# Performance work log

Measured on AMD Instinct MI355X. Metric: run time of the kernel, lower is better.

## Reference

```python
import jax, jax.numpy as jnp
import numpy as np

N = 16384
C_IN = 128
C_OUT = 128
S_DIM = 4
P_DIM = 32
K = 16


def setup_inputs() -> dict:
    key = jax.random.key(0)
    ks = jax.random.split(key, 8)
    lim = lambda fan_in: 1.0 / np.sqrt(fan_in)
    u = lambda k_, shape, b: jax.random.uniform(k_, shape, jnp.float32, -b, b)
    return {
        "x": jax.random.normal(ks[0], (N, C_IN), jnp.float32),
        "Ws": u(ks[1], (S_DIM, C_IN), lim(C_IN)),
        "bs": u(ks[2], (S_DIM,), lim(C_IN)),
        "Wh": u(ks[3], (P_DIM, C_IN), lim(C_IN)),
        "bh": u(ks[4], (P_DIM,), lim(C_IN)),
        "W1": u(ks[5], (C_OUT, C_IN), lim(C_IN)),
        "W2": u(ks[6], (C_OUT, 2 * P_DIM), lim(2 * P_DIM)),
        "b2": u(ks[7], (C_OUT,), lim(2 * P_DIM)),
        "k": K,
    }


def reference(x, Ws, bs, Wh, bh, W1, W2, b2, k):
    # latent space positions and message vectors
    s = x @ Ws.T + bs            # [N, S]
    h = x @ Wh.T + bh            # [N, P]
    # squared-distance matrix via Gram trick (monotone in true distance,
    # so k-NN indices match torch.cdist + topk(largest=False))
    sq = jnp.sum(s * s, axis=-1)                         # [N]
    d2 = sq[:, None] + sq[None, :] - 2.0 * (s @ s.T)     # [N, N]
    _, idx = jax.lax.top_k(-d2, k)                       # [N, k] neighbour ids (incl. self)
    # exact squared latent distance to selected neighbours (as in torch code)
    s_j = s[idx]                                          # [N, k, S]
    w = jnp.exp(-10.0 * jnp.sum((s[:, None, :] - s_j) ** 2, axis=-1))  # [N, k]
    msg = h[idx] * w[..., None]                           # [N, k, P]
    agg = jnp.concatenate([msg.mean(axis=1), msg.max(axis=1)], axis=-1)  # [N, 2P]
    return x @ W1.T + agg @ W2.T + b2                     # [N, C_OUT]
```

## Files before the change

### kernel.cpp

```cpp
#include <hip/hip_runtime.h>
#include <hip/hip_bf16.h>


#define NPTS 16384
#define CIN  128
#define SD   4
#define PD   32
#define KNN  16
#define COUT 128
#define FLTMAX 3.4028234663852886e+38f
#define NBIN 33
#define QPB  8
#define QCAP 512
#define MCAP 128
#define EPAD 1e-3f

typedef float v2f __attribute__((ext_vector_type(2)));
typedef unsigned int uint;
typedef unsigned long long u64;
typedef unsigned short u16;
typedef __attribute__((ext_vector_type(8))) short bf16x8;
typedef __attribute__((ext_vector_type(4))) float f32x4;

#define WS_S4     0
#define WS_H      0x40000
#define WS_AGG_M  0x280000
#define WS_SA     0x280000
#define WS_SB     0x300000
#define WS_WT_M   0x680000
#define WS_T2     0x6A0000
#define WS_MASK   0x700000
#define WS_NEED_M 0x2700000
#define WS_CJ_F   0x400000
#define WS_AGG_F  0xC00000
#define WS_WT_F   0x1000000
#define JS   16
#define TJF  (NPTS/JS)

__device__ __forceinline__ float d2f(const float4 a, const float4 b) {
  v2f d0 = {a.x - b.x, a.y - b.y};
  v2f d1 = {a.z - b.z, a.w - b.w};
  v2f pr = d0*d0 + d1*d1;
  return pr.x + pr.y;
}

__device__ __forceinline__ u16 f2bf(float x) {
  uint u = __float_as_uint(x);
  uint r = (u + 0x7FFFu + ((u >> 16) & 1u)) >> 16;
  return (u16)r;
}
__device__ __forceinline__ float bf2f(u16 h) {
  return __uint_as_float(((uint)h) << 16);
}

__global__ __launch_bounds__(256) void k1_proj(
    const float* __restrict__ x, const float* __restrict__ Ws, const float* __restrict__ bs,
    const float* __restrict__ Wh, const float* __restrict__ bh,
    float4* __restrict__ s4, float* __restrict__ h) {
  __shared__ float  lw[36*128];
  __shared__ float  lx[64*132];
  __shared__ double rs[3*64*5];
  __shared__ float  rh[3*64*33];
  const int t = threadIdx.x;
  const int row0 = blockIdx.x * 64;
  for (int i2 = t; i2 < 36*128; i2 += 256)
    lw[i2] = (i2 < 512) ? Ws[i2] : Wh[i2 - 512];
#pragma unroll
  for (int g = 0; g < 8; ++g) {
    int fi = g*256 + t;
    int r = fi >> 5, c4 = fi & 31;
    *(float4*)&lx[r*132 + c4*4] = *(const float4*)&x[(size_t)(row0 + r)*CIN + c4*4];
  }
  __syncthreads();
  const int kq = t >> 6;
  const int r  = t & 63;
  const int kb = kq * 32;
  double sacc[4] = {0.0, 0.0, 0.0, 0.0};
  float  hacc[32];
#pragma unroll
  for (int p = 0; p < 32; ++p) hacc[p] = 0.f;
#pragma unroll
  for (int k4 = 0; k4 < 8; ++k4) {
    float4 xv = *(const float4*)&lx[r*132 + kb + k4*4];
    int kg = kb + k4*4;
#pragma unroll
    for (int p = 0; p < 4; ++p) {
      float4 wv = *(const float4*)&lw[p*128 + kg];
      sacc[p] = fma((double)xv.x, (double)wv.x, sacc[p]);
      sacc[p] = fma((double)xv.y, (double)wv.y, sacc[p]);
      sacc[p] = fma((double)xv.z, (double)wv.z, sacc[p]);
      sacc[p] = fma((double)xv.w, (double)wv.w, sacc[p]);
    }
#pragma unroll
    for (int p = 0; p < 32; ++p) {
      float4 wv = *(const float4*)&lw[(4+p)*128 + kg];
      hacc[p] = fmaf(xv.x, wv.x, fmaf(xv.y, wv.y, fmaf(xv.z, wv.z, fmaf(xv.w, wv.w, hacc[p]))));
    }
  }
  if (kq > 0) {
    const int bq = kq - 1;
#pragma unroll
    for (int d = 0; d < 4; ++d) rs[(bq*64 + r)*5 + d] = sacc[d];
#pragma unroll
    for (int p = 0; p < 32; ++p) rh[(bq*64 + r)*33 + p] = hacc[p];
  }
  __syncthreads();
  if (kq == 0) {
    const int row = row0 + r;
    float so[4];
#pragma unroll
    for (int d = 0; d < 4; ++d) {
      double sd = sacc[d] + rs[(0*64 + r)*5 + d] + rs[(1*64 + r)*5 + d]
                + rs[(2*64 + r)*5 + d] + (double)bs[d];
      so[d] = (float)sd;
    }
    s4[row] = make_float4(so[0], so[1], so[2], so[3]);
#pragma unroll
    for (int p4 = 0; p4 < 8; ++p4) {
      float o[4];
#pragma unroll
      for (int c = 0; c < 4; ++c) {
        int p = p4*4 + c;
        o[c] = hacc[p] + rh[(0*64 + r)*33 + p] + rh[(1*64 + r)*33 + p]
             + rh[(2*64 + r)*33 + p] + bh[p];
      }
      *(float4*)&h[(size_t)row*PD + p4*4] = make_float4(o[0], o[1], o[2], o[3]);
    }
  }
}

__global__ __launch_bounds__(256) void k2t_thresh(
    const float4* __restrict__ s4, float* __restrict__ t2) {
  __shared__ float4 tile[2064];
  __shared__ uint   lhist[256*NBIN];
  const int t = threadIdx.x;
#pragma unroll
  for (int g = 0; g < 8; ++g) {
    int j = g*256 + t;
    tile[j + (j >> 7)] = s4[j];
  }
#pragma unroll
  for (int b = 0; b < NBIN; ++b) lhist[t*NBIN + b] = 0u;
  const int ql = t >> 4, tq = t & 15;
  const int q  = blockIdx.x*16 + ql;
  const float4 sq = s4[q];
  __syncthreads();
  float tau = d2f(sq, tile[tq*129]);
#pragma unroll
  for (int m = 1; m < 16; m <<= 1) tau = fmaxf(tau, __shfl_xor(tau, m, 16));
  const int ktop = (int)(__float_as_uint(tau) >> 21);
  const int hb = t*NBIN;
#pragma unroll 4
  for (int u = 0; u < 128; ++u) {
    float4 p = tile[tq*129 + u];
    float e = d2f(sq, p);
    int key = (int)(__float_as_uint(e) >> 21);
    int rel = ktop - key;
    rel = rel < 0 ? 0 : (rel > 32 ? 32 : rel);
    atomicAdd(&lhist[hb + rel], 1u);
  }
  __syncthreads();
  uint c0 = 0, c1 = 0;
  const int qb = ql*16;
  for (int u = 0; u < 16; ++u) {
    c0 += lhist[(qb + u)*NBIN + tq*2];
    c1 += (tq*2 + 1 < NBIN) ? lhist[(qb + u)*NBIN + tq*2 + 1] : 0u;
  }
  int S = (int)(c0 + c1);
#pragma unroll
  for (int d = 1; d < 16; d <<= 1) {
    int v = __shfl_down(S, d, 16);
    S += (tq + d < 16) ? v : 0;
  }
  int g = -1;
  if (S >= KNN) g = 2*tq;
  if (S - (int)c0 >= KNN) g = 2*tq + 1;
#pragma unroll
  for (int m = 1; m < 16; m <<= 1) g = max(g, __shfl_xor(g, m, 16));
  if (tq == 0) {
    uint K = (uint)(ktop - g);
    t2[q] = __uint_as_float((K << 21) | 0x1FFFFFu);
  }
}

__global__ __launch_bounds__(256) void k1b_pack(
    const float4* __restrict__ s4, const float* __restrict__ t2,
    uint4* __restrict__ sA, uint4* __restrict__ sB) {
  const int i = blockIdx.x*256 + threadIdx.x;
  const float4 s = s4[i];
  float sv[4] = {s.x, s.y, s.z, s.w};
  const float n2 = s.x*s.x + s.y*s.y + s.z*s.z + s.w*s.w;
  u16 hb[4], lb[4];
#pragma unroll
  for (int d = 0; d < 4; ++d) {
    u16 hh = f2bf(sv[d]);
    hb[d] = hh;
    lb[d] = f2bf(sv[d] - bf2f(hh));
  }
  const float aq = -0.5f*(n2 - t2[i]) + EPAD;
  const float bn = -0.5f*n2;
  u16 aqh = f2bf(aq); u16 aql = f2bf(aq - bf2f(aqh));
  u16 bnh = f2bf(bn); u16 bnl = f2bf(bn - bf2f(bnh));
  const uint oneone = 0x3F803F80u;
  uint a0 = (uint)hb[0] | ((uint)hb[1] << 16);
  uint a1 = (uint)hb[2] | ((uint)hb[3] << 16);
  uint l0 = (uint)lb[0] | ((uint)lb[1] << 16);
  uint l1 = (uint)lb[2] | ((uint)lb[3] << 16);
  uint aqw = (uint)aqh | ((uint)aql << 16);
  uint bnw = (uint)bnh | ((uint)bnl << 16);
  uint4 A0; A0.x = a0; A0.y = a1; A0.z = a0; A0.w = a1;
  uint4 A1; A1.x = l0; A1.y = l1; A1.z = oneone; A1.w = aqw;
  uint4 B0; B0.x = a0; B0.y = a1; B0.z = l0; B0.w = l1;
  uint4 B1; B1.x = a0; B1.y = a1; B1.z = bnw; B1.w = oneone;
  sA[(size_t)i*2]     = A0;
  sA[(size_t)i*2 + 1] = A1;
  sB[(size_t)i*2]     = B0;
  sB[(size_t)i*2 + 1] = B1;
}

__global__ __launch_bounds__(256) void k2b_mfma(
    const u16* __restrict__ sA, const u16* __restrict__ sB, uint4* __restrict__ maskw) {
  __shared__ u16 lB[1024*16];
  const int t  = threadIdx.x;
  const int wv = t >> 6, ln = t & 63;
  const int lr = ln & 15, lk = ln >> 4;
  const int qb = (blockIdx.x >> 4) * 256 + wv * 64;
  const int j0 = (blockIdx.x & 15) * 1024;
  for (int r = t; r < 1024; r += 256) {
    const uint4* src = (const uint4*)&sB[(size_t)(j0 + r)*16];
    uint4 v0 = src[0], v1 = src[1];
    *(uint4*)&lB[r*16]     = v0;
    *(uint4*)&lB[r*16 + 8] = v1;
  }
  const bf16x8 zf = {0,0,0,0,0,0,0,0};
  bf16x8 afr[4];
#pragma unroll
  for (int m = 0; m < 4; ++m)
    afr[m] = (lk < 2) ? *(const bf16x8*)&sA[(size_t)(qb + m*16 + lr)*16 + lk*8] : zf;
  __syncthreads();
  const int mg   = lk;
  const int isel = lr & 3;
  const int g16  = (lr >> 2) * 16;
#pragma unroll 1
  for (int cc = 0; cc < 8; ++cc) {
    uint mw[4] = {0u, 0u, 0u, 0u};
#pragma unroll
    for (int jt = 0; jt < 8; ++jt) {
      const bf16x8 bfr = (lk < 2) ? *(const bf16x8*)&lB[(cc*128 + jt*16 + lr)*16 + lk*8] : zf;
#pragma unroll
      for (int m = 0; m < 4; ++m) {
        f32x4 acc = {0.f, 0.f, 0.f, 0.f};
        acc = __builtin_amdgcn_mfma_f32_16x16x32_bf16(afr[m], bfr, acc, 0, 0, 0);
        u64 b0 = __ballot(acc[0] >= 0.f);
        u64 b1 = __ballot(acc[1] >= 0.f);
        u64 b2 = __ballot(acc[2] >= 0.f);
        u64 b3 = __ballot(acc[3] >= 0.f);
        u64 bb = (isel == 0) ? b0 : (isel == 1) ? b1 : (isel == 2) ? b2 : b3;
        uint piece = (uint)(bb >> g16) & 0xFFFFu;
        piece = (mg == m) ? piece : 0u;
        mw[jt >> 1] |= piece << (16 * (jt & 1));
      }
    }
    const int c = (blockIdx.x & 15) * 8 + cc;
    uint4 o; o.x = mw[0]; o.y = mw[1]; o.z = mw[2]; o.w = mw[3];
    maskw[(size_t)c*NPTS + qb + ln] = o;
  }
}

__global__ __launch_bounds__(256) void k3_sel2(
    const float4* __restrict__ s4, const float* __restrict__ h,
    const uint4* __restrict__ maskw, float* __restrict__ agg) {
  __shared__ u64  qbuf[QPB*MCAP];
  __shared__ u64  keys[QPB*QCAP];
  __shared__ u64  win[QPB*KNN];
  __shared__ uint hist[QPB*32];
  __shared__ uint cnts[QPB];
  __shared__ uint mc[QPB];
  unsigned short* jl = (unsigned short*)qbuf;
  const int t  = threadIdx.x;
  const int ql = t >> 5, ln = t & 31;
  const int q  = blockIdx.x*QPB + ql;
  if (ln == 0) { cnts[ql] = 0u; mc[ql] = 0u; }
  hist[ql*32 + ln] = 0u;
  if (ln < KNN) win[ql*KNN + ln] = 0ull;
  const float4 sq = s4[q];
  __syncthreads();
  const int qa = t & 7;
  const int cg = t >> 3;
  uint wv[16]; int pc = 0;
#pragma unroll
  for (int u = 0; u < 4; ++u) {
    const int c = cg + u*32;
    uint4 m4 = maskw[(size_t)c*NPTS + blockIdx.x*QPB + qa];
    wv[u*4+0] = m4.x; wv[u*4+1] = m4.y; wv[u*4+2] = m4.z; wv[u*4+3] = m4.w;
    pc += __popc(m4.x) + __popc(m4.y) + __popc(m4.z) + __popc(m4.w);
  }
  int base = (int)atomicAdd(&cnts[qa], (uint)pc);
#pragma unroll
  for (int w = 0; w < 16; ++w) {
    uint bits = wv[w];
    const int jb = (cg + (w >> 2)*32)*128 + (w & 3)*32;
    while (bits) {
      int b = __builtin_ctz(bits); bits &= bits - 1;
      if (base < QCAP) jl[qa*QCAP + base] = (unsigned short)(jb + b);
      ++base;
    }
  }
  __syncthreads();
  const int cnt = min((int)cnts[ql], QCAP);
  uint kmax = 0u;
  for (int u = ln; u < cnt; u += 32) {
    int j = jl[ql*QCAP + u];
    float e = d2f(sq, s4[j]);
    uint db = __float_as_uint(e);
    keys[ql*QCAP + u] = ((u64)db << 14) | (uint)j;
    kmax = max(kmax, db >> 21);
  }
#pragma unroll
  for (int m = 1; m < 32; m <<= 1) kmax = max(kmax, (uint)__shfl_xor((int)kmax, m, 32));
  for (int u = ln; u < cnt; u += 32) {
    uint cls = (uint)(keys[ql*QCAP + u] >> 35);
    uint rel = min(kmax - cls, 31u);
    atomicAdd(&hist[ql*32 + rel], 1u);
  }
  __syncthreads();
  uint cum = hist[ql*32 + ln];
#pragma unroll
  for (int d = 1; d < 32; d <<= 1) {
    uint v = (uint)__shfl_down((int)cum, d, 32);
    if (ln + d < 32) cum += v;
  }
  const uint need = (uint)(cnt < KNN ? cnt : KNN);
  u64 bal = __ballot(cum >= need);
  uint half = (uint)(bal >> (((t >> 5) & 1) * 32));
  const uint rstar = 31u - (uint)__builtin_clz(half);
  const uint bcls = kmax - rstar;
  __syncthreads();
  for (int u = ln; u < cnt; u += 32) {
    u64 key = keys[ql*QCAP + u];
    if ((uint)(key >> 35) <= bcls) {
      uint pos = atomicAdd(&mc[ql], 1u);
      if (pos < MCAP) qbuf[ql*MCAP + pos] = key;
    }
  }
  __syncthreads();
  const int mcnt = (int)mc[ql];
  if (mcnt <= MCAP) {
    for (int w = ln; w < mcnt; w += 32) {
      u64 key = qbuf[ql*MCAP + w];
      int rank = 0;
      for (int v = 0; v < mcnt; ++v) rank += (qbuf[ql*MCAP + v] < key) ? 1 : 0;
      if (rank < KNN) win[ql*KNN + rank] = key;
    }
  } else {
    for (int u = ln; u < cnt; u += 32) {
      u64 key = keys[ql*QCAP + u];
      if ((uint)(key >> 35) <= bcls) {
        int rank = 0;
        for (int v = 0; v < cnt; ++v) rank += (keys[ql*QCAP + v] < key) ? 1 : 0;
        if (rank < KNN) win[ql*KNN + rank] = key;
      }
    }
  }
  __syncthreads();
  float sum = 0.f, mx = -FLTMAX;
#pragma unroll 1
  for (int r = 0; r < KNN; ++r) {
    u64 key = win[ql*KNN + r];
    float d2 = __uint_as_float((uint)(key >> 14));
    int j = (int)(key & 16383u);
    float w = __expf(-10.f * d2);
    float m = w * h[(size_t)j*PD + ln];
    sum += m; mx = fmaxf(mx, m);
  }
  agg[(size_t)q*64 + ln]      = sum * 0.0625f;
  agg[(size_t)q*64 + 32 + ln] = mx;
}

__global__ __launch_bounds__(256) void k2_knn_fb(
    const float4* __restrict__ s4, unsigned short* __restrict__ cand_j) {
  __shared__ float4 tile[TJF];
  __shared__ int    lbuf[256*33];
  const int t  = threadIdx.x;
  const int ib = blockIdx.x & 31;
  const int jc = blockIdx.x >> 5;
  const int jbase = jc * TJF;
#pragma unroll
  for (int g = 0; g < 4; ++g) tile[g*256 + t] = s4[jbase + g*256 + t];
  const int ia = ib*256 + t;
  const int ic = ia + 8192;
  const float4 sa = s4[ia];
  const float4 sc = s4[ic];
  __syncthreads();
  float va[KNN], vb[KNN]; int ja[KNN], jb[KNN];
#pragma unroll
  for (int q = 0; q < KNN; ++q) { va[q] = FLTMAX; ja[q] = 0; vb[q] = FLTMAX; jb[q] = 0; }
  float cma = FLTMAX, cmb = FLTMAX;
  int cpa = 0, cpb = 0, ca = 0, cb = 0;
  auto insertA = [&](float e, int jj) {
#pragma unroll
    for (int q = 0; q < KNN; ++q) if (q == cpa) { va[q] = e; ja[q] = jj; }
    cma = va[0]; cpa = 0;
#pragma unroll
    for (int q = 1; q < KNN; ++q) { if (va[q] > cma) { cma = va[q]; cpa = q; } }
  };
  auto insertB = [&](float e, int jj) {
#pragma unroll
    for (int q = 0; q < KNN; ++q) if (q == cpb) { vb[q] = e; jb[q] = jj; }
    cmb = vb[0]; cpb = 0;
#pragma unroll
    for (int q = 1; q < KNN; ++q) { if (vb[q] > cmb) { cmb = vb[q]; cpb = q; } }
  };
  auto compactA = [&]() {
    for (int u = 0; u < ca; ++u) {
      int jj = lbuf[t*33 + u];
      float e = d2f(sa, tile[jj]);
      if (e < cma) insertA(e, jj);
    }
    ca = 0;
  };
  auto compactB = [&]() {
    for (int u = 0; u < cb; ++u) {
      int jj = lbuf[t*33 + 16 + u];
      float e = d2f(sc, tile[jj]);
      if (e < cmb) insertB(e, jj);
    }
    cb = 0;
  };
  for (int ob = 0; ob < TJF/8; ++ob) {
#pragma unroll
    for (int u = 0; u < 8; ++u) {
      int jj = ob*8 + u;
      float4 p = tile[jj];
      float ea = d2f(sa, p);
      float eb = d2f(sc, p);
      if (ea < cma) { lbuf[t*33 + ca] = jj; ++ca; }
      if (eb < cmb) { lbuf[t*33 + 16 + cb] = jj; ++cb; }
    }
    if (__any(ca > 8)) compactA();
    if (__any(cb > 8)) compactB();
  }
  compactA(); compactB();
#pragma unroll
  for (int q = 0; q < KNN; ++q) {
    int c = jc*KNN + q;
    cand_j[(size_t)c*NPTS + ia] = (unsigned short)(ja[q] + jbase);
    cand_j[(size_t)c*NPTS + ic] = (unsigned short)(jb[q] + jbase);
  }
}

__global__ __launch_bounds__(256) void k3_merge_fb(
    const float4* __restrict__ s4, const float4* __restrict__ h4,
    const unsigned short* __restrict__ cand_j, float* __restrict__ agg) {
  __shared__ float le[64*67];
  __shared__ int   lj[64*67];
  const int t  = threadIdx.x;
  const int il = t & 63, tq = t >> 6;
  const int i  = blockIdx.x*64 + il;
  const float4 si = s4[i];
  float val[KNN]; int vid[KNN];
#pragma unroll
  for (int q = 0; q < KNN; ++q) { val[q] = FLTMAX; vid[q] = 0; }
  float cmax = FLTMAX; int cpos = 0;
  for (int u = 0; u < 64; ++u) {
    int c = tq*64 + u;
    int j = cand_j[(size_t)c*NPTS + i];
    float e = d2f(si, s4[j]);
    if (e < cmax) {
#pragma unroll
      for (int q = 0; q < KNN; ++q) if (q == cpos) { val[q] = e; vid[q] = j; }
      cmax = val[0]; cpos = 0;
#pragma unroll
      for (int q = 1; q < KNN; ++q) { if (val[q] > cmax) { cmax = val[q]; cpos = q; } }
    }
  }
#pragma unroll
  for (int q = 0; q < KNN; ++q) {
    le[il*67 + tq*16 + q] = val[q];
    lj[il*67 + tq*16 + q] = vid[q];
  }
  __syncthreads();
  if (t < 64) {
    float mv[KNN]; int mj[KNN];
#pragma unroll
    for (int q = 0; q < KNN; ++q) { mv[q] = FLTMAX; mj[q] = 0; }
    float cm2 = FLTMAX; int cp2 = 0;
    for (int u = 0; u < 64; ++u) {
      float e = le[t*67 + u];
      int   j = lj[t*67 + u];
      if (e < cm2) {
#pragma unroll
        for (int q = 0; q < KNN; ++q) if (q == cp2) { mv[q] = e; mj[q] = j; }
        cm2 = mv[0]; cp2 = 0;
#pragma unroll
        for (int q = 1; q < KNN; ++q) { if (mv[q] > cm2) { cm2 = mv[q]; cp2 = q; } }
      }
    }
#pragma unroll
    for (int q = 0; q < KNN; ++q) {
      le[t*67 + q] = __expf(-10.f * mv[q]);
      lj[t*67 + q] = mj[q];
    }
  }
  __syncthreads();
  float ms[8], mm[8];
#pragma unroll
  for (int p = 0; p < 8; ++p) { ms[p] = 0.f; mm[p] = -FLTMAX; }
#pragma unroll 1
  for (int q = 0; q < KNN; ++q) {
    float w = le[il*67 + q];
    int   j = lj[il*67 + q];
    float4 a = h4[(size_t)j*8 + tq*2];
    float4 b = h4[(size_t)j*8 + tq*2 + 1];
    float m0 = a.x*w, m1 = a.y*w, m2 = a.z*w, m3 = a.w*w;
    float m4 = b.x*w, m5 = b.y*w, m6 = b.z*w, m7 = b.w*w;
    ms[0] += m0; mm[0] = fmaxf(mm[0], m0);
    ms[1] += m1; mm[1] = fmaxf(mm[1], m1);
    ms[2] += m2; mm[2] = fmaxf(mm[2], m2);
    ms[3] += m3; mm[3] = fmaxf(mm[3], m3);
    ms[4] += m4; mm[4] = fmaxf(mm[4], m4);
    ms[5] += m5; mm[5] = fmaxf(mm[5], m5);
    ms[6] += m6; mm[6] = fmaxf(mm[6], m6);
    ms[7] += m7; mm[7] = fmaxf(mm[7], m7);
  }
  float4 o0 = make_float4(ms[0]*0.0625f, ms[1]*0.0625f, ms[2]*0.0625f, ms[3]*0.0625f);
  float4 o1 = make_float4(ms[4]*0.0625f, ms[5]*0.0625f, ms[6]*0.0625f, ms[7]*0.0625f);
  *(float4*)&agg[(size_t)i*64 + tq*8]      = o0;
  *(float4*)&agg[(size_t)i*64 + tq*8 + 4]  = o1;
  *(float4*)&agg[(size_t)i*64 + 32 + tq*8]     = make_float4(mm[0], mm[1], mm[2], mm[3]);
  *(float4*)&agg[(size_t)i*64 + 32 + tq*8 + 4] = make_float4(mm[4], mm[5], mm[6], mm[7]);
}

__global__ __launch_bounds__(256) void k4a_wt(
    const float* __restrict__ W1, const float* __restrict__ W2, float* __restrict__ wT) {
  int idx = blockIdx.x*256 + threadIdx.x;
  if (idx >= 192*COUT) return;
  int k = idx >> 7, c = idx & 127;
  float v = (k < 128) ? W1[(size_t)c*128 + k] : W2[(size_t)c*64 + (k - 128)];
  wT[(size_t)k*COUT + c] = v;
}

__global__ __launch_bounds__(256) void k4_out2(
    const float* __restrict__ x, const float* __restrict__ agg,
    const float* __restrict__ wT, const float* __restrict__ b2,
    float* __restrict__ out) {
  __shared__ float xa[32*192];
  const int t = threadIdx.x;
  const int row0 = blockIdx.x * 32;
#pragma unroll
  for (int g = 0; g < 4; ++g) {
    int fi = g*256 + t;
    int r = fi >> 5, c4 = fi & 31;
    *(float4*)&xa[r*192 + c4*4] = *(const float4*)&x[(size_t)(row0+r)*CIN + c4*4];
  }
#pragma unroll
  for (int g = 0; g < 2; ++g) {
    int fi = g*256 + t;
    int r = fi >> 4, c4 = fi & 15;
    *(float4*)&xa[r*192 + 128 + c4*4] = *(const float4*)&agg[(size_t)(row0+r)*64 + c4*4];
  }
  __syncthreads();
  const int c4 = t & 31;
  const int rg = t >> 5;
  float acc[4][4];
#pragma unroll
  for (int r = 0; r < 4; ++r) { acc[r][0]=0.f; acc[r][1]=0.f; acc[r][2]=0.f; acc[r][3]=0.f; }
  for (int k = 0; k < 192; k += 4) {
    float4 w0 = *(const float4*)&wT[(size_t)(k+0)*COUT + c4*4];
    float4 w1 = *(const float4*)&wT[(size_t)(k+1)*COUT + c4*4];
    float4 w2 = *(const float4*)&wT[(size_t)(k+2)*COUT + c4*4];
    float4 w3 = *(const float4*)&wT[(size_t)(k+3)*COUT + c4*4];
#pragma unroll
    for (int r = 0; r < 4; ++r) {
      float4 xv = *(const float4*)&xa[(rg*4 + r)*192 + k];
      acc[r][0] = fmaf(xv.x, w0.x, fmaf(xv.y, w1.x, fmaf(xv.z, w2.x, fmaf(xv.w, w3.x, acc[r][0]))));
      acc[r][1] = fmaf(xv.x, w0.y, fmaf(xv.y, w1.y, fmaf(xv.z, w2.y, fmaf(xv.w, w3.y, acc[r][1]))));
      acc[r][2] = fmaf(xv.x, w0.z, fmaf(xv.y, w1.z, fmaf(xv.z, w2.z, fmaf(xv.w, w3.z, acc[r][2]))));
      acc[r][3] = fmaf(xv.x, w0.w, fmaf(xv.y, w1.w, fmaf(xv.z, w2.w, fmaf(xv.w, w3.w, acc[r][3]))));
    }
  }
  float4 bias = *(const float4*)&b2[c4*4];
#pragma unroll
  for (int r = 0; r < 4; ++r) {
    float4 o = make_float4(acc[r][0]+bias.x, acc[r][1]+bias.y, acc[r][2]+bias.z, acc[r][3]+bias.w);
    *(float4*)&out[(size_t)(row0 + rg*4 + r)*COUT + c4*4] = o;
  }
}

extern "C" void kernel_launch(void* const* d_in, const int* in_sizes, int n_in,
                              void* d_out, int out_size, void* d_ws, size_t ws_size,
                              hipStream_t stream) {
  const float* x  = (const float*)d_in[0];
  const float* Ws = (const float*)d_in[1];
  const float* bs = (const float*)d_in[2];
  const float* Wh = (const float*)d_in[3];
  const float* bh = (const float*)d_in[4];
  const float* W1 = (const float*)d_in[5];
  const float* W2 = (const float*)d_in[6];
  const float* b2 = (const float*)d_in[7];
  float* out = (float*)d_out;

  char* ws = (char*)d_ws;
  float4* s4 = (float4*)(ws + WS_S4);
  float*  h  = (float*) (ws + WS_H);

  k1_proj<<<NPTS/64, 256, 0, stream>>>(x, Ws, bs, Wh, bh, s4, h);

  if (ws_size >= (size_t)WS_NEED_M) {
    float* t2  = (float*)(ws + WS_T2);
    float* agg = (float*)(ws + WS_AGG_M);
    float* wT  = (float*)(ws + WS_WT_M);
    uint4* sa  = (uint4*)(ws + WS_SA);
    uint4* sb  = (uint4*)(ws + WS_SB);
    uint4* mw  = (uint4*)(ws + WS_MASK);
    k2t_thresh<<<NPTS/16, 256, 0, stream>>>(s4, t2);
    k1b_pack<<<NPTS/256, 256, 0, stream>>>(s4, t2, sa, sb);
    k2b_mfma<<<1024, 256, 0, stream>>>((const u16*)sa, (const u16*)sb, mw);
    k3_sel2<<<NPTS/QPB, 256, 0, stream>>>(s4, h, (const uint4*)mw, agg);
    k4a_wt<<<(192*COUT + 255)/256, 256, 0, stream>>>(W1, W2, wT);
    k4_out2<<<NPTS/32, 256, 0, stream>>>(x, agg, wT, b2, out);
  } else {
    unsigned short* cj = (unsigned short*)(ws + WS_CJ_F);
    float* agg = (float*)(ws + WS_AGG_F);
    float* wT  = (float*)(ws + WS_WT_F);
    k2_knn_fb<<<512, 256, 0, stream>>>(s4, cj);
    k3_merge_fb<<<NPTS/64, 256, 0, stream>>>(s4, (const float4*)h, cj, agg);
    k4a_wt<<<(192*COUT + 255)/256, 256, 0, stream>>>(W1, W2, wT);
    k4_out2<<<NPTS/32, 256, 0, stream>>>(x, agg, wT, b2, out);
  }
}
```

Measured before the change: 224.9 us.

## Use 32x32x16 MFMA with per-lane bit packing for kNN candidate masks

Rewrites the mask-building kernel to use 32x32x16 bf16 MFMAs with the candidate tile as A and queries as B. Sign bits come straight from each lane's 16 accumulator values by bit packing plus one cross-half shuffle, instead of four ballots per 16x16 MFMA. This removes the wasted half of the K=32 inputs that were zero-padded, and most of the ballot and select overhead. The catch is a more complex accumulator layout whose bit ordering has to match the old mask format exactly.

```diff
diff --git a/kernel.cpp b/kernel.cpp
--- a/kernel.cpp
+++ b/kernel.cpp
@@ -21,6 +21,7 @@
 typedef unsigned short u16;
 typedef __attribute__((ext_vector_type(8))) short bf16x8;
 typedef __attribute__((ext_vector_type(4))) float f32x4;
+typedef __attribute__((ext_vector_type(16))) float f32x16;
 
 #define WS_S4     0
 #define WS_H      0x40000
@@ -218,52 +219,59 @@
   sB[(size_t)i*2 + 1] = B1;
 }
 
+__device__ __forceinline__ uint packbits16(const f32x16 a, const int shft) {
+  uint b[4];
+#pragma unroll
+  for (int g = 0; g < 4; ++g) {
+    uint bg = 0u;
+#pragma unroll
+    for (int e = 3; e >= 0; --e)
+      bg = bg + bg + ((~__float_as_uint(a[4*g + e])) >> 31);
+    b[g] = bg;
+  }
+  return (b[0] | (b[1] << 8) | (b[2] << 16) | (b[3] << 24)) << shft;
+}
+
 __global__ __launch_bounds__(256) void k2b_mfma(
     const u16* __restrict__ sA, const u16* __restrict__ sB, uint4* __restrict__ maskw) {
   __shared__ u16 lB[1024*16];
-  const int t  = threadIdx.x;
-  const int wv = t >> 6, ln = t & 63;
-  const int lr = ln & 15, lk = ln >> 4;
-  const int qb = (blockIdx.x >> 4) * 256 + wv * 64;
-  const int j0 = (blockIdx.x & 15) * 1024;
+  const int t   = threadIdx.x;
+  const int wv  = t >> 6, ln = t & 63;
+  const int l31 = ln & 31, hi = ln >> 5;
+  const int qbase = (blockIdx.x >> 4) * 256 + wv * 64;
+  const int j0    = (blockIdx.x & 15) * 1024;
   for (int r = t; r < 1024; r += 256) {
     const uint4* src = (const uint4*)&sB[(size_t)(j0 + r)*16];
     uint4 v0 = src[0], v1 = src[1];
     *(uint4*)&lB[r*16]     = v0;
     *(uint4*)&lB[r*16 + 8] = v1;
   }
-  const bf16x8 zf = {0,0,0,0,0,0,0,0};
-  bf16x8 afr[4];
-#pragma unroll
-  for (int m = 0; m < 4; ++m)
-    afr[m] = (lk < 2) ? *(const bf16x8*)&sA[(size_t)(qb + m*16 + lr)*16 + lk*8] : zf;
-  __syncthreads();
-  const int mg   = lk;
-  const int isel = lr & 3;
-  const int g16  = (lr >> 2) * 16;
+  const bf16x8 qf0 = *(const bf16x8*)&sA[(size_t)(qbase + l31)*16 + hi*8];
+  const bf16x8 qf1 = *(const bf16x8*)&sA[(size_t)(qbase + 32 + l31)*16 + hi*8];
+  __syncthreads();
+  const int sh = hi * 4;
+  const f32x16 zc = {0.f,0.f,0.f,0.f,0.f,0.f,0.f,0.f,0.f,0.f,0.f,0.f,0.f,0.f,0.f,0.f};
 #pragma unroll 1
   for (int cc = 0; cc < 8; ++cc) {
-    uint mw[4] = {0u, 0u, 0u, 0u};
-#pragma unroll
-    for (int jt = 0; jt < 8; ++jt) {
-      const bf16x8 bfr = (lk < 2) ? *(const bf16x8*)&lB[(cc*128 + jt*16 + lr)*16 + lk*8] : zf;
-#pragma unroll
-      for (int m = 0; m < 4; ++m) {
-        f32x4 acc = {0.f, 0.f, 0.f, 0.f};
-        acc = __builtin_amdgcn_mfma_f32_16x16x32_bf16(afr[m], bfr, acc, 0, 0, 0);
-        u64 b0 = __ballot(acc[0] >= 0.f);
-        u64 b1 = __ballot(acc[1] >= 0.f);
-        u64 b2 = __ballot(acc[2] >= 0.f);
-        u64 b3 = __ballot(acc[3] >= 0.f);
-        u64 bb = (isel == 0) ? b0 : (isel == 1) ? b1 : (isel == 2) ? b2 : b3;
-        uint piece = (uint)(bb >> g16) & 0xFFFFu;
-        piece = (mg == m) ? piece : 0u;
-        mw[jt >> 1] |= piece << (16 * (jt & 1));
-      }
-    }
-    const int c = (blockIdx.x & 15) * 8 + cc;
-    uint4 o; o.x = mw[0]; o.y = mw[1]; o.z = mw[2]; o.w = mw[3];
-    maskw[(size_t)c*NPTS + qb + ln] = o;
+    uint w0[4], w1[4];
+#pragma unroll
+    for (int jt = 0; jt < 4; ++jt) {
+      const bf16x8 af = *(const bf16x8*)&lB[(cc*128 + jt*32 + l31)*16 + hi*8];
+      f32x16 a0 = __builtin_amdgcn_mfma_f32_32x32x16_bf16(af, qf0, zc, 0, 0, 0);
+      f32x16 a1 = __builtin_amdgcn_mfma_f32_32x32x16_bf16(af, qf1, zc, 0, 0, 0);
+      w0[jt] = packbits16(a0, sh);
+      w1[jt] = packbits16(a1, sh);
+    }
+    uint of[4];
+#pragma unroll
+    for (int jt = 0; jt < 4; ++jt) {
+      uint f0 = w0[jt] | (uint)__shfl_xor((int)w0[jt], 32);
+      uint f1 = w1[jt] | (uint)__shfl_xor((int)w1[jt], 32);
+      of[jt] = hi ? f1 : f0;
+    }
+    const int c = (blockIdx.x & 15)*8 + cc;
+    uint4 o; o.x = of[0]; o.y = of[1]; o.z = of[2]; o.w = of[3];
+    maskw[(size_t)c*NPTS + qbase + ln] = o;
   }
 }
 
```

After: 207.9 us. 1.08x faster.
